# Kernel optimization log

Hardware: AMD Instinct MI355X
Metric: run time of the kernel (lower is better)

The kernel has to match this reference:

```python
import jax, jax.numpy as jnp
import numpy as np

EPS = 1e-6        # RMSNorm140 eps
LAM = 0.1         # lambda_: second-order score weight
HAD = 0.05        # hadamard_scale

def _rmsnorm(x, w):
    return x * jax.lax.rsqrt(jnp.mean(x * x, axis=-1, keepdims=True) + EPS) * w

def _rope(x):
    # x: [b, h, s, d]; interleaved-pair rotary embedding (theta=10000)
    b, h, s, d = x.shape
    inv = 1.0 / (10000.0 ** (jnp.arange(0, d, 2, dtype=jnp.float32) / d))
    ang = jnp.arange(s, dtype=jnp.float32)[:, None] * inv[None, :]  # [s, d/2]
    cos, sin = jnp.cos(ang), jnp.sin(ang)
    x1, x2 = x[..., 0::2], x[..., 1::2]
    out = jnp.stack([x1 * cos - x2 * sin, x1 * sin + x2 * cos], axis=-1)
    return out.reshape(b, h, s, d)

def _rotate_half(x):
    d = x.shape[-1] // 2
    return jnp.concatenate([-x[..., d:], x[..., :d]], axis=-1)

def _attn_pass(Q, K, V):
    # scores = (Q@K^T + lam * Q^2 @ (K^2)^T) / sqrt(head_dim)   (second-order amplify)
    scale = 1.0 / jnp.sqrt(jnp.float32(Q.shape[-1]))
    scores = (jnp.einsum('bhsd,bhtd->bhst', Q, K)
              + LAM * jnp.einsum('bhsd,bhtd->bhst', Q * Q, K * K)) * scale
    return jnp.einsum('bhst,bhtd->bhsd', jax.nn.softmax(scores, axis=-1), V)

def _attention(x, wq, wk, wv, wo, gate_w):
    b, s, dim = x.shape
    hd = gate_w.shape[0]
    nh = dim // hd
    def proj(w):  # StickyLinear: x @ W^T, W stored [out, in]
        return (x @ w.T).reshape(b, s, nh, hd).transpose(0, 2, 1, 3)  # [b,h,s,d]
    Q, K, V = proj(wq), proj(wk), proj(wv)
    Q, K = _rope(Q), _rope(K)
    out1 = _attn_pass(Q, K, V)
    # rotated second pass + per-channel sigmoid gate over head_dim
    out2 = _attn_pass(_rotate_half(Q), _rotate_half(K), V)
    g = jax.nn.sigmoid(gate_w)
    out = out1 * (1.0 - g) + out2 * g
    out = out + HAD * out * out  # Hadamard mix (elementwise nonlinearity)
    out = out.transpose(0, 2, 1, 3).reshape(b, s, dim)
    return out @ wo.T

def _ffn(x, w1, w3, w2):
    # SwiGLU: down( silu(gate(x)) * up(x) )
    return (jax.nn.silu(x @ w1.T) * (x @ w3.T)) @ w2.T

def reference(x, norm1_w, norm2_w, wq, wk, wv, wo, gate_w, w1, w3, w2):
    h = x + _attention(_rmsnorm(x, norm1_w), wq, wk, wv, wo, gate_w)
    return h + _ffn(_rmsnorm(h, norm2_w), w1, w3, w2)

def setup_inputs() -> dict:
    B, S, D, NH, DFF = 2, 1024, 2048, 16, 8192
    HD = D // NH
    key = jax.random.key(0)
    ks = jax.random.split(key, 9)
    std = 0.02
    return {
        'x': jax.random.normal(ks[0], (B, S, D), dtype=jnp.float32),
        'norm1_w': jnp.ones((D,), jnp.float32),
        'norm2_w': jnp.ones((D,), jnp.float32),
        'wq': jax.random.normal(ks[1], (D, D), jnp.float32) * std,
        'wk': jax.random.normal(ks[2], (D, D), jnp.float32) * std,
        'wv': jax.random.normal(ks[3], (D, D), jnp.float32) * std,
        'wo': jax.random.normal(ks[4], (D, D), jnp.float32) * std,
        'gate_w': jax.random.normal(ks[5], (HD,), jnp.float32) * 0.01,
        'w1': jax.random.normal(ks[6], (DFF, D), jnp.float32) * std,
        'w3': jax.random.normal(ks[7], (DFF, D), jnp.float32) * std,
        'w2': jax.random.normal(ks[8], (D, DFF), jnp.float32) * std,
    }
```

## Files before the change

kernel.cpp:

```cpp
#include <hip/hip_runtime.h>
#include <hip/hip_bf16.h>

typedef unsigned short u16;
typedef unsigned int u32;
typedef u16 u16x8 __attribute__((ext_vector_type(8)));
typedef float f32x4 __attribute__((ext_vector_type(4)));

__device__ __forceinline__ u16 f2bf(float f) {
  union { float f; u32 u; } v; v.f = f;
  u32 r = v.u + 0x7FFFu + ((v.u >> 16) & 1u);
  return (u16)(r >> 16);
}
__device__ __forceinline__ float bf2f(u16 h) {
  union { u32 u; float f; } v; v.u = ((u32)h) << 16;
  return v.f;
}
__device__ __forceinline__ void mfma_bf16_16x16x32(f32x4& acc, const f32x4& a, const f32x4& b) {
  asm("v_mfma_f32_16x16x32_bf16 %0, %1, %2, %0" : "+v"(acc) : "v"(a), "v"(b));
}
__device__ __forceinline__ void gload_lds16(const void* g, void* l) {
  __builtin_amdgcn_global_load_lds(
      (const __attribute__((address_space(1))) unsigned int*)g,
      (__attribute__((address_space(3))) unsigned int*)l, 16, 0, 0);
}

__global__ __launch_bounds__(256) void cvt_k(const float* __restrict__ src,
                                             u16* __restrict__ dst, int n8) {
  int i = blockIdx.x * 256 + threadIdx.x;
  if (i >= n8) return;
  float4 f0 = *(const float4*)&src[(size_t)i * 8];
  float4 f1 = *(const float4*)&src[(size_t)i * 8 + 4];
  u16x8 o;
  o[0] = f2bf(f0.x); o[1] = f2bf(f0.y); o[2] = f2bf(f0.z); o[3] = f2bf(f0.w);
  o[4] = f2bf(f1.x); o[5] = f2bf(f1.y); o[6] = f2bf(f1.z); o[7] = f2bf(f1.w);
  *(u16x8*)&dst[(size_t)i * 8] = o;
}

__global__ __launch_bounds__(256) void cvt13_k(const float* __restrict__ src,
                                               u16* __restrict__ dst, int half) {
  int r = blockIdx.x;
  int dr = ((r >> 4) << 5) + (r & 15) + (half << 4);
  int t = threadIdx.x;
  const float* s = src + (size_t)r * 2048 + t * 8;
  float4 f0 = *(const float4*)s;
  float4 f1 = *(const float4*)(s + 4);
  u16x8 o;
  o[0] = f2bf(f0.x); o[1] = f2bf(f0.y); o[2] = f2bf(f0.z); o[3] = f2bf(f0.w);
  o[4] = f2bf(f1.x); o[5] = f2bf(f1.y); o[6] = f2bf(f1.z); o[7] = f2bf(f1.w);
  *(u16x8*)&dst[(size_t)dr * 2048 + t * 8] = o;
}

__global__ __launch_bounds__(256) void rmsnorm_k(const float* __restrict__ X,
                                                 const float* __restrict__ W,
                                                 u16* __restrict__ O) {
  const int row = blockIdx.x;
  const int tid = threadIdx.x;
  const float* x = X + (size_t)row * 2048;
  float4 v0 = *(const float4*)&x[tid * 8];
  float4 v1 = *(const float4*)&x[tid * 8 + 4];
  float s = v0.x * v0.x + v0.y * v0.y + v0.z * v0.z + v0.w * v0.w
          + v1.x * v1.x + v1.y * v1.y + v1.z * v1.z + v1.w * v1.w;
  #pragma unroll
  for (int m = 1; m < 64; m <<= 1) s += __shfl_xor(s, m);
  __shared__ float red[4];
  if ((tid & 63) == 0) red[tid >> 6] = s;
  __syncthreads();
  float tot = red[0] + red[1] + red[2] + red[3];
  float r = rsqrtf(tot * (1.0f / 2048.0f) + 1e-6f);
  float4 w0 = *(const float4*)&W[tid * 8];
  float4 w1 = *(const float4*)&W[tid * 8 + 4];
  u16x8 o;
  o[0] = f2bf(v0.x * r * w0.x); o[1] = f2bf(v0.y * r * w0.y);
  o[2] = f2bf(v0.z * r * w0.z); o[3] = f2bf(v0.w * r * w0.w);
  o[4] = f2bf(v1.x * r * w1.x); o[5] = f2bf(v1.y * r * w1.y);
  o[6] = f2bf(v1.z * r * w1.z); o[7] = f2bf(v1.w * r * w1.w);
  *(u16x8*)&O[(size_t)row * 2048 + tid * 8] = o;
}

#define EPI_F32 0
#define EPI_ADDF32 1
#define EPI_SWIGLU 2
#define EPI_BF16G 3

template <int EPI>
__global__ __launch_bounds__(256) void gemm_bt(const u16* __restrict__ A,
                                               const u16* __restrict__ B,
                                               float* __restrict__ Cf,
                                               u16* __restrict__ Cb,
                                               const float* __restrict__ R,
                                               int M, int N, int Kt,
                                               int lda, int ldb) {
  __shared__ __align__(16) u16 As[2][128 * 32];
  __shared__ __align__(16) u16 Bs[2][128 * 32];
  const int tid = threadIdx.x;
  const int lane = tid & 63;
  const int w = tid >> 6;
  const int wm = w >> 1, wn = w & 1;
  const int m0 = blockIdx.y * 128, n0 = blockIdx.x * 128;
  const int z = blockIdx.z;
  A += (size_t)z * Kt;
  B += (size_t)z * Kt;
  Cf += (size_t)z * M * N;
  const int r0 = tid >> 2;
  const int c0 = (tid & 3) * 8;
  const int r1 = r0 + 64;
  const int laneM = lane & 15;
  const int laneK = (lane >> 4) * 8;

  f32x4 acc[4][4];
  #pragma unroll
  for (int i = 0; i < 4; i++)
    #pragma unroll
    for (int j = 0; j < 4; j++) acc[i][j] = (f32x4){0.f, 0.f, 0.f, 0.f};

  const u16* Ar0 = &A[(size_t)(m0 + r0) * lda + c0];
  const u16* Ar1 = &A[(size_t)(m0 + r1) * lda + c0];
  const u16* Br0 = &B[(size_t)(n0 + r0) * ldb + c0];
  const u16* Br1 = &B[(size_t)(n0 + r1) * ldb + c0];
  const int lofs0 = r0 * 32 + c0;
  const int lofs1 = r1 * 32 + c0;

  auto stage = [&](int bsel, int kt) {
    gload_lds16(Ar0 + kt, &As[bsel][lofs0]);
    gload_lds16(Ar1 + kt, &As[bsel][lofs1]);
    gload_lds16(Br0 + kt, &Bs[bsel][lofs0]);
    gload_lds16(Br1 + kt, &Bs[bsel][lofs1]);
  };

  stage(0, 0);
  const int nt = Kt >> 5;
  for (int t = 0; t < nt; t++) {
    const int cur = t & 1;
    if (t + 1 < nt) {
      stage(cur ^ 1, (t + 1) << 5);
      asm volatile("s_waitcnt vmcnt(4)" ::: "memory");
    } else {
      asm volatile("s_waitcnt vmcnt(0)" ::: "memory");
    }
    __builtin_amdgcn_s_barrier();
    f32x4 af[4], bfr[4];
    #pragma unroll
    for (int mi = 0; mi < 4; mi++)
      af[mi] = *(const f32x4*)&As[cur][(wm * 64 + mi * 16 + laneM) * 32 + laneK];
    #pragma unroll
    for (int ni = 0; ni < 4; ni++)
      bfr[ni] = *(const f32x4*)&Bs[cur][(wn * 64 + ni * 16 + laneM) * 32 + laneK];
    #pragma unroll
    for (int mi = 0; mi < 4; mi++)
      #pragma unroll
      for (int ni = 0; ni < 4; ni++)
        mfma_bf16_16x16x32(acc[mi][ni], af[mi], bfr[ni]);
    __builtin_amdgcn_s_barrier();
  }

  const int rowb = (lane >> 4) * 4;
  const int coll = lane & 15;
  #pragma unroll
  for (int mi = 0; mi < 4; mi++) {
    #pragma unroll
    for (int i = 0; i < 4; i++) {
      int row = m0 + wm * 64 + mi * 16 + rowb + i;
      #pragma unroll
      for (int ni = 0; ni < 4; ni++) {
        int col = n0 + wn * 64 + ni * 16 + coll;
        size_t idx = (size_t)row * N + col;
        float v = acc[mi][ni][i];
        if constexpr (EPI == EPI_F32) Cf[idx] = v;
        else Cf[idx] = v + R[idx];
      }
    }
  }
}

template <int EPI>
__global__ __launch_bounds__(512, 2) void gemm256(const u16* __restrict__ A,
                                                  const u16* __restrict__ B,
                                                  float* __restrict__ Cf,
                                                  u16* __restrict__ Cb,
                                                  int M, int N, int Kt,
                                                  int lda, int ldb) {
  __shared__ __align__(16) char sm[131072];
  const int tid = threadIdx.x;
  const int lane = tid & 63, w = tid >> 6;
  const int wr = w >> 2, wc = w & 3;
  const int laneM = lane & 15, laneG = lane >> 4;
  const int m0 = blockIdx.y * 256, n0 = blockIdx.x * 256;
  const int z = blockIdx.z;
  A += (size_t)z * Kt;
  B += (size_t)z * Kt;
  Cf += (size_t)z * M * N;

  const int srow = tid >> 3;
  const int scb = (tid & 7) * 16;

  f32x4 acc[8][4];
  #pragma unroll
  for (int i = 0; i < 8; i++)
    #pragma unroll
    for (int j = 0; j < 4; j++) acc[i][j] = (f32x4){0.f, 0.f, 0.f, 0.f};

  auto stage = [&](int buf, int ktE, int ht) {
    const int half = ht & 1;
    const bool isA = ht < 2;
    char* base = sm + (isA ? 0 : 65536) + buf * 32768 + half * 16384;
    const u16* src = isA ? A : B;
    const int ld = isA ? lda : ldb;
    const int rb = (isA ? m0 : n0) + half * 128;
    #pragma unroll
    for (int j = 0; j < 2; j++) {
      int row = j * 64 + srow;
      int scol = (scb ^ ((row & 7) << 4)) >> 1;
      gload_lds16(src + (size_t)(rb + row) * ld + ktE + scol,
                  base + j * 8192 + tid * 16);
    }
  };

  const int nkt = Kt >> 6;
  #pragma unroll
  for (int ht = 0; ht < 4; ht++) stage(0, 0, ht);

  const int bHalf = wc >> 1;
  const int bRow0 = (wc & 1) * 64;

  for (int t = 0; t < nkt; t++) {
    const int cb_ = t & 1;
    char* aBase = sm + cb_ * 32768 + wr * 16384;
    char* bBase = sm + 65536 + cb_ * 32768 + bHalf * 16384;
    const bool pre = (t + 1 < nkt);
    const int ktE1 = (t + 1) << 6;

    if (pre) {
      #pragma unroll
      for (int ht = 0; ht < 4; ht++) stage(cb_ ^ 1, ktE1, ht);
      asm volatile("s_waitcnt vmcnt(8)" ::: "memory");
    } else {
      asm volatile("s_waitcnt vmcnt(0)" ::: "memory");
    }
    __builtin_amdgcn_s_barrier();
    __builtin_amdgcn_s_setprio(1);

    f32x4 af[4][2], bg[4][2];
    #pragma unroll
    for (int ni = 0; ni < 4; ni++)
      #pragma unroll
      for (int ks = 0; ks < 2; ks++) {
        int r = bRow0 + ni * 16 + laneM;
        int cbv = ks * 64 + laneG * 16;
        bg[ni][ks] = *(const f32x4*)(bBase + r * 128 + (cbv ^ ((r & 7) << 4)));
      }
    #pragma unroll
    for (int mi = 0; mi < 4; mi++)
      #pragma unroll
      for (int ks = 0; ks < 2; ks++) {
        int r = mi * 16 + laneM;
        int cbv = ks * 64 + laneG * 16;
        af[mi][ks] = *(const f32x4*)(aBase + r * 128 + (cbv ^ ((r & 7) << 4)));
      }
    #pragma unroll
    for (int mi = 0; mi < 4; mi++)
      #pragma unroll
      for (int ni = 0; ni < 4; ni++)
        #pragma unroll
        for (int ks = 0; ks < 2; ks++)
          mfma_bf16_16x16x32(acc[mi][ni], af[mi][ks], bg[ni][ks]);
    #pragma unroll
    for (int mi = 0; mi < 4; mi++)
      #pragma unroll
      for (int ks = 0; ks < 2; ks++) {
        int r = (4 + mi) * 16 + laneM;
        int cbv = ks * 64 + laneG * 16;
        af[mi][ks] = *(const f32x4*)(aBase + r * 128 + (cbv ^ ((r & 7) << 4)));
      }
    #pragma unroll
    for (int mi = 0; mi < 4; mi++)
      #pragma unroll
      for (int ni = 0; ni < 4; ni++)
        #pragma unroll
        for (int ks = 0; ks < 2; ks++)
          mfma_bf16_16x16x32(acc[4 + mi][ni], af[mi][ks], bg[ni][ks]);

    __builtin_amdgcn_s_setprio(0);
    __builtin_amdgcn_s_barrier();
  }

  #pragma unroll
  for (int mi = 0; mi < 8; mi++) {
    #pragma unroll
    for (int i = 0; i < 4; i++) {
      int row = m0 + wr * 128 + mi * 16 + laneG * 4 + i;
      if constexpr (EPI == EPI_SWIGLU) {
        #pragma unroll
        for (int np = 0; np < 2; np++) {
          float g = acc[mi][np * 2][i];
          float u = acc[mi][np * 2 + 1][i];
          float sg = g / (1.0f + __expf(-g));
          int j = (n0 >> 1) + wc * 32 + np * 16 + laneM;
          Cb[(size_t)row * (N >> 1) + j] = f2bf(sg * u);
        }
      } else if constexpr (EPI == EPI_BF16G) {
        #pragma unroll
        for (int ni = 0; ni < 4; ni++) {
          int col = n0 + wc * 64 + ni * 16 + laneM;
          Cb[(size_t)row * N + col] = f2bf(acc[mi][ni][i]);
        }
      } else {
        #pragma unroll
        for (int ni = 0; ni < 4; ni++) {
          int col = n0 + wc * 64 + ni * 16 + laneM;
          Cf[(size_t)row * N + col] = acc[mi][ni][i];
        }
      }
    }
  }
}

__global__ __launch_bounds__(256) void reduce5_k(const float* __restrict__ P,
                                                 const float* __restrict__ H,
                                                 float* __restrict__ out) {
  size_t i = ((size_t)blockIdx.x * 256 + threadIdx.x) * 4;
  const size_t MN = 4194304;
  float4 a = *(const float4*)&P[i];
  float4 b = *(const float4*)&P[MN + i];
  float4 c = *(const float4*)&P[2 * MN + i];
  float4 d = *(const float4*)&P[3 * MN + i];
  float4 h = *(const float4*)&H[i];
  float4 o;
  o.x = a.x + b.x + c.x + d.x + h.x;
  o.y = a.y + b.y + c.y + d.y + h.y;
  o.z = a.z + b.z + c.z + d.z + h.z;
  o.w = a.w + b.w + c.w + d.w + h.w;
  *(float4*)&out[i] = o;
}

__device__ __forceinline__ void rope_row(const u16* __restrict__ src,
                                         u16* __restrict__ dst, int s, int q4) {
  float vv[32];
  #pragma unroll
  for (int t = 0; t < 4; t++) {
    u16x8 v = *(const u16x8*)&src[t * 8];
    #pragma unroll
    for (int j = 0; j < 8; j++) vv[t * 8 + j] = bf2f(v[j]);
  }
  u16 o1[32], o2[32];
  #pragma unroll
  for (int jl = 0; jl < 16; jl++) {
    int j = q4 * 16 + jl;
    float inv = exp2f(-(float)j * 0.20762050593046014f);
    float ang = (float)s * inv;
    float sn, cs;
    __sincosf(ang, &sn, &cs);
    float a = vv[2 * jl], b = vv[2 * jl + 1];
    float r1 = a * cs - b * sn;
    float r2 = a * sn + b * cs;
    o1[2 * jl] = f2bf(r1);
    o1[2 * jl + 1] = f2bf(r2);
    o2[2 * jl] = f2bf(0.31622776601683794f * r1 * r1);
    o2[2 * jl + 1] = f2bf(0.31622776601683794f * r2 * r2);
  }
  #pragma unroll
  for (int t = 0; t < 4; t++) {
    *(u16x8*)&dst[q4 * 32 + t * 8] = *(const u16x8*)&o1[t * 8];
    *(u16x8*)&dst[128 + q4 * 32 + t * 8] = *(const u16x8*)&o2[t * 8];
  }
}

__global__ __launch_bounds__(256) void qkv_post_k(const u16* __restrict__ QKVB,
                                                  u16* __restrict__ Qe,
                                                  u16* __restrict__ Ke,
                                                  u16* __restrict__ Vt) {
  const int st = blockIdx.x;
  const int bh = blockIdx.y;
  const int b = bh >> 4, h = bh & 15;
  const int tid = threadIdx.x;
  {
    int r = tid >> 2, q4 = tid & 3;
    int s = st * 64 + r;
    size_t rowin = ((size_t)b * 1024 + s) * 6144 + h * 128 + q4 * 32;
    size_t rowe = ((size_t)bh * 1024 + s) * 256;
    rope_row(QKVB + rowin, Qe + rowe, s, q4);
    rope_row(QKVB + rowin + 2048, Ke + rowe, s, q4);
  }
  __shared__ __align__(16) u16 vts[128 * 72];
  {
    int r = tid >> 2, q4 = tid & 3;
    int s = st * 64 + r;
    const u16* src = QKVB + ((size_t)b * 1024 + s) * 6144 + 4096 + h * 128 + q4 * 32;
    #pragma unroll
    for (int k = 0; k < 32; k += 8) {
      u16x8 v = *(const u16x8*)&src[k];
      int d = q4 * 32 + k;
      #pragma unroll
      for (int j = 0; j < 8; j++) vts[(d + j) * 72 + r] = v[j];
    }
  }
  __syncthreads();
  {
    int d = tid >> 1, sp = (tid & 1) * 32;
    u16* dst = Vt + ((size_t)bh * 128 + d) * 1024 + st * 64 + sp;
    #pragma unroll
    for (int k = 0; k < 32; k += 8)
      *(u16x8*)&dst[k] = *(const u16x8*)&vts[d * 72 + sp + k];
  }
}

__global__ __launch_bounds__(256, 2) void attn_k(const u16* __restrict__ Qe,
                                                 const u16* __restrict__ Ke,
                                                 const u16* __restrict__ Vt,
                                                 u16* __restrict__ AO) {
  const int bh = blockIdx.x;
  const int qt = blockIdx.y;
  const int b = bh >> 4, h = bh & 15;
  const int tid = threadIdx.x;
  const int w = tid >> 6, lane = tid & 63;
  const int laneM = lane & 15, laneG = lane >> 4;

  __shared__ __align__(16) char smem[57344];
  u16* plu = (u16*)(smem + 49152 + w * 2048);

  const char* KeB = (const char*)Ke + (size_t)bh * 524288;
  const char* VtB = (const char*)Vt + (size_t)bh * 262144;

  const size_t qbase = ((size_t)bh * 1024 + qt * 64 + w * 16 + laneM) * 256 + laneG * 8;
  f32x4 qf[8];
  #pragma unroll
  for (int kk = 0; kk < 8; kk++) qf[kk] = *(const f32x4*)&Qe[qbase + kk * 32];

  float m_i[4], l_i[4];
  #pragma unroll
  for (int i = 0; i < 4; i++) { m_i[i] = -1e30f; l_i[i] = 0.f; }
  f32x4 accO[8];
  #pragma unroll
  for (int n = 0; n < 8; n++) accO[n] = (f32x4){0.f, 0.f, 0.f, 0.f};

  u16x8 kreg[4], vreg[2];
  auto loadRegs = [&](int ktn) {
    const char* ks = KeB + (size_t)ktn * 16384;
    #pragma unroll
    for (int j = 0; j < 4; j++) {
      int p = j * 4096 + tid * 16;
      kreg[j] = *(const u16x8*)(ks + p);
    }
    const char* vs = VtB + (size_t)ktn * 64;
    #pragma unroll
    for (int j = 0; j < 2; j++) {
      int p = j * 4096 + tid * 16;
      int r = p >> 6, x = p & 63;
      vreg[j] = *(const u16x8*)(vs + (size_t)r * 2048 + x);
    }
  };
  auto writeLDS = [&](int bsel) {
    char* kd = smem + (bsel ? 16384 : 0);
    #pragma unroll
    for (int j = 0; j < 4; j++) {
      int p = j * 4096 + tid * 16;
      int r = p >> 9, x = p & 511;
      *(u16x8*)(kd + r * 512 + (x ^ ((r & 7) << 4))) = kreg[j];
    }
    char* vd = smem + 32768 + (bsel ? 8192 : 0);
    #pragma unroll
    for (int j = 0; j < 2; j++) {
      int p = j * 4096 + tid * 16;
      int r = p >> 6, x = p & 63;
      *(u16x8*)(vd + r * 64 + (x ^ (((r >> 1) & 3) << 4))) = vreg[j];
    }
  };

  loadRegs(0);
  writeLDS(0);
  int cur = 0;
  const float scale = 0.08838834764831845f;

  for (int kt = 0; kt < 32; kt++) {
    if (kt < 31) loadRegs(kt + 1);
    __syncthreads();
    const char* Kc = smem + (cur ? 16384 : 0);
    const char* Vc = smem + 32768 + (cur ? 8192 : 0);

    f32x4 accS[2];
    #pragma unroll
    for (int n = 0; n < 2; n++) accS[n] = (f32x4){0.f, 0.f, 0.f, 0.f};
    #pragma unroll
    for (int n = 0; n < 2; n++) {
      int r = n * 16 + laneM;
      const char* krow = Kc + r * 512;
      int sw = (r & 7) << 4;
      #pragma unroll
      for (int kk = 0; kk < 8; kk++) {
        f32x4 kf = *(const f32x4*)(krow + ((kk * 64 + laneG * 16) ^ sw));
        mfma_bf16_16x16x32(accS[n], qf[kk], kf);
      }
    }

    float p[2][4], sf[4];
    #pragma unroll
    for (int i = 0; i < 4; i++) {
      float mx = fmaxf(accS[0][i], accS[1][i]) * scale;
      #pragma unroll
      for (int m = 1; m < 16; m <<= 1) mx = fmaxf(mx, __shfl_xor(mx, m));
      float mnew = fmaxf(m_i[i], mx);
      sf[i] = __expf(m_i[i] - mnew);
      m_i[i] = mnew;
      float p0 = __expf(accS[0][i] * scale - mnew);
      float p1 = __expf(accS[1][i] * scale - mnew);
      p[0][i] = p0; p[1][i] = p1;
      float rs = p0 + p1;
      #pragma unroll
      for (int m = 1; m < 16; m <<= 1) rs += __shfl_xor(rs, m);
      l_i[i] = l_i[i] * sf[i] + rs;
    }
    #pragma unroll
    for (int n = 0; n < 8; n++) {
      accO[n][0] *= sf[0]; accO[n][1] *= sf[1];
      accO[n][2] *= sf[2]; accO[n][3] *= sf[3];
    }

    #pragma unroll
    for (int n = 0; n < 2; n++)
      #pragma unroll
      for (int i = 0; i < 4; i++) {
        int row = laneG * 4 + i;
        int col = n * 16 + laneM;
        plu[row * 64 + (col ^ (((row >> 2) & 3) << 4))] = f2bf(p[n][i]);
      }
    f32x4 pa = *(const f32x4*)&plu[laneM * 64 +
                                   ((laneG * 8) ^ (((laneM >> 2) & 3) << 4))];

    #pragma unroll
    for (int n = 0; n < 8; n++) {
      int r = n * 16 + laneM;
      f32x4 vf = *(const f32x4*)(Vc + r * 64 + ((laneG * 16) ^ (((r >> 1) & 3) << 4)));
      mfma_bf16_16x16x32(accO[n], pa, vf);
    }

    if (kt < 31) writeLDS(cur ^ 1);
    cur ^= 1;
  }

  #pragma unroll
  for (int i = 0; i < 4; i++) {
    float inv_l = 1.f / l_i[i];
    int row = b * 1024 + qt * 64 + w * 16 + laneG * 4 + i;
    #pragma unroll
    for (int n = 0; n < 8; n++) {
      float o = accO[n][i] * inv_l;
      o = o + 0.05f * o * o;
      AO[(size_t)row * 2048 + h * 128 + n * 16 + laneM] = f2bf(o);
    }
  }
}

extern "C" void kernel_launch(void* const* d_in, const int* in_sizes, int n_in,
                              void* d_out, int out_size, void* d_ws, size_t ws_size,
                              hipStream_t stream) {
  const float* x   = (const float*)d_in[0];
  const float* n1w = (const float*)d_in[1];
  const float* n2w = (const float*)d_in[2];
  const float* wq  = (const float*)d_in[3];
  const float* wk  = (const float*)d_in[4];
  const float* wv  = (const float*)d_in[5];
  const float* wo  = (const float*)d_in[6];
  const float* w1  = (const float*)d_in[8];
  const float* w3  = (const float*)d_in[9];
  const float* w2  = (const float*)d_in[10];

  char* ws = (char*)d_ws;
  u16* WQKVb = (u16*)(ws + 0);
  u16* WOb   = (u16*)(ws + 25165824);
  u16* W13b  = (u16*)(ws + 33554432);
  u16* W2b   = (u16*)(ws + 100663296);
  u16* XN    = (u16*)(ws + 134217728);
  u16* QKVB  = (u16*)(ws + 142606336);
  u16* U     = (u16*)(ws + 142606336);
  float* P   = (float*)(ws + 176160768);
  u16* QE    = (u16*)(ws + 192937984);
  u16* KE    = (u16*)(ws + 209715200);
  u16* VT    = (u16*)(ws + 226492416);
  u16* AO    = (u16*)(ws + 234881024);
  float* H   = (float*)(ws + 243269632);

  cvt_k<<<2048, 256, 0, stream>>>(wq, WQKVb, 524288);
  cvt_k<<<2048, 256, 0, stream>>>(wk, WQKVb + 4194304, 524288);
  cvt_k<<<2048, 256, 0, stream>>>(wv, WQKVb + 8388608, 524288);
  cvt_k<<<2048, 256, 0, stream>>>(wo, WOb, 524288);
  cvt13_k<<<8192, 256, 0, stream>>>(w1, W13b, 0);
  cvt13_k<<<8192, 256, 0, stream>>>(w3, W13b, 1);
  cvt_k<<<8192, 256, 0, stream>>>(w2, W2b, 2097152);

  rmsnorm_k<<<2048, 256, 0, stream>>>(x, n1w, XN);

  gemm256<EPI_BF16G><<<dim3(24, 8), 512, 0, stream>>>(
      XN, WQKVb, nullptr, QKVB, 2048, 6144, 2048, 2048, 2048);

  qkv_post_k<<<dim3(16, 32), 256, 0, stream>>>(QKVB, QE, KE, VT);

  attn_k<<<dim3(32, 16), 256, 0, stream>>>(QE, KE, VT, AO);

  gemm_bt<EPI_ADDF32><<<dim3(16, 16), 256, 0, stream>>>(
      AO, WOb, H, nullptr, x, 2048, 2048, 2048, 2048, 2048);

  rmsnorm_k<<<2048, 256, 0, stream>>>(H, n2w, XN);

  gemm256<EPI_SWIGLU><<<dim3(64, 8), 512, 0, stream>>>(
      XN, W13b, nullptr, U, 2048, 16384, 2048, 2048, 2048);

  gemm256<EPI_F32><<<dim3(8, 8, 4), 512, 0, stream>>>(
      U, W2b, P, nullptr, 2048, 2048, 2048, 8192, 8192);

  reduce5_k<<<4096, 256, 0, stream>>>(P, H, (float*)d_out);
}
```

Baseline: 499.1 us.

## Merge weight-conversion launches and split gemm256 prefetch across compute halves

```diff
diff --git a/kernel.cpp b/kernel.cpp
--- a/kernel.cpp
+++ b/kernel.cpp
@@ -24,30 +24,46 @@
       (__attribute__((address_space(3))) unsigned int*)l, 16, 0, 0);
 }
 
+__device__ __forceinline__ u16x8 cvt_row8(const float* p) {
+  float4 f0 = *(const float4*)p;
+  float4 f1 = *(const float4*)(p + 4);
+  u16x8 o;
+  o[0] = f2bf(f0.x); o[1] = f2bf(f0.y); o[2] = f2bf(f0.z); o[3] = f2bf(f0.w);
+  o[4] = f2bf(f1.x); o[5] = f2bf(f1.y); o[6] = f2bf(f1.z); o[7] = f2bf(f1.w);
+  return o;
+}
+
 __global__ __launch_bounds__(256) void cvt_k(const float* __restrict__ src,
                                              u16* __restrict__ dst, int n8) {
   int i = blockIdx.x * 256 + threadIdx.x;
   if (i >= n8) return;
-  float4 f0 = *(const float4*)&src[(size_t)i * 8];
-  float4 f1 = *(const float4*)&src[(size_t)i * 8 + 4];
-  u16x8 o;
-  o[0] = f2bf(f0.x); o[1] = f2bf(f0.y); o[2] = f2bf(f0.z); o[3] = f2bf(f0.w);
-  o[4] = f2bf(f1.x); o[5] = f2bf(f1.y); o[6] = f2bf(f1.z); o[7] = f2bf(f1.w);
-  *(u16x8*)&dst[(size_t)i * 8] = o;
-}
-
-__global__ __launch_bounds__(256) void cvt13_k(const float* __restrict__ src,
-                                               u16* __restrict__ dst, int half) {
-  int r = blockIdx.x;
+  *(u16x8*)&dst[(size_t)i * 8] = cvt_row8(&src[(size_t)i * 8]);
+}
+
+__global__ __launch_bounds__(256) void cvt4_k(const float* __restrict__ s0,
+                                              const float* __restrict__ s1,
+                                              const float* __restrict__ s2,
+                                              const float* __restrict__ s3,
+                                              u16* __restrict__ dst) {
+  int bid = blockIdx.x;
+  const float* s = (bid < 2048) ? s0 : (bid < 4096) ? s1 : (bid < 6144) ? s2 : s3;
+  int r = bid & 2047;
+  int t = threadIdx.x;
+  *(u16x8*)&dst[(size_t)bid * 2048 + t * 8] =
+      cvt_row8(s + (size_t)r * 2048 + t * 8);
+}
+
+__global__ __launch_bounds__(256) void cvt13_2(const float* __restrict__ w1,
+                                               const float* __restrict__ w3,
+                                               u16* __restrict__ dst) {
+  int bid = blockIdx.x;
+  int half = bid >> 13;
+  int r = bid & 8191;
+  const float* s = half ? w3 : w1;
   int dr = ((r >> 4) << 5) + (r & 15) + (half << 4);
   int t = threadIdx.x;
-  const float* s = src + (size_t)r * 2048 + t * 8;
-  float4 f0 = *(const float4*)s;
-  float4 f1 = *(const float4*)(s + 4);
-  u16x8 o;
-  o[0] = f2bf(f0.x); o[1] = f2bf(f0.y); o[2] = f2bf(f0.z); o[3] = f2bf(f0.w);
-  o[4] = f2bf(f1.x); o[5] = f2bf(f1.y); o[6] = f2bf(f1.z); o[7] = f2bf(f1.w);
-  *(u16x8*)&dst[(size_t)dr * 2048 + t * 8] = o;
+  *(u16x8*)&dst[(size_t)dr * 2048 + t * 8] =
+      cvt_row8(s + (size_t)r * 2048 + t * 8);
 }
 
 __global__ __launch_bounds__(256) void rmsnorm_k(const float* __restrict__ X,
@@ -229,17 +245,12 @@
     const bool pre = (t + 1 < nkt);
     const int ktE1 = (t + 1) << 6;
 
-    if (pre) {
-      #pragma unroll
-      for (int ht = 0; ht < 4; ht++) stage(cb_ ^ 1, ktE1, ht);
-      asm volatile("s_waitcnt vmcnt(8)" ::: "memory");
-    } else {
-      asm volatile("s_waitcnt vmcnt(0)" ::: "memory");
-    }
+    f32x4 af[4][2], bg[4][2];
+
+    if (pre) { stage(cb_ ^ 1, ktE1, 0); stage(cb_ ^ 1, ktE1, 1); }
+    if (pre) asm volatile("s_waitcnt vmcnt(4)" ::: "memory");
+    else     asm volatile("s_waitcnt vmcnt(0)" ::: "memory");
     __builtin_amdgcn_s_barrier();
-    __builtin_amdgcn_s_setprio(1);
-
-    f32x4 af[4][2], bg[4][2];
     #pragma unroll
     for (int ni = 0; ni < 4; ni++)
       #pragma unroll
@@ -256,6 +267,9 @@
         int cbv = ks * 64 + laneG * 16;
         af[mi][ks] = *(const f32x4*)(aBase + r * 128 + (cbv ^ ((r & 7) << 4)));
       }
+    asm volatile("s_waitcnt lgkmcnt(0)" ::: "memory");
+    __builtin_amdgcn_sched_barrier(0);
+    __builtin_amdgcn_s_setprio(1);
     #pragma unroll
     for (int mi = 0; mi < 4; mi++)
       #pragma unroll
@@ -263,6 +277,11 @@
         #pragma unroll
         for (int ks = 0; ks < 2; ks++)
           mfma_bf16_16x16x32(acc[mi][ni], af[mi][ks], bg[ni][ks]);
+    __builtin_amdgcn_s_setprio(0);
+    __builtin_amdgcn_sched_barrier(0);
+
+    if (pre) { stage(cb_ ^ 1, ktE1, 2); stage(cb_ ^ 1, ktE1, 3); }
+    __builtin_amdgcn_s_barrier();
     #pragma unroll
     for (int mi = 0; mi < 4; mi++)
       #pragma unroll
@@ -271,6 +290,9 @@
         int cbv = ks * 64 + laneG * 16;
         af[mi][ks] = *(const f32x4*)(aBase + r * 128 + (cbv ^ ((r & 7) << 4)));
       }
+    asm volatile("s_waitcnt lgkmcnt(0)" ::: "memory");
+    __builtin_amdgcn_sched_barrier(0);
+    __builtin_amdgcn_s_setprio(1);
     #pragma unroll
     for (int mi = 0; mi < 4; mi++)
       #pragma unroll
@@ -278,8 +300,8 @@
         #pragma unroll
         for (int ks = 0; ks < 2; ks++)
           mfma_bf16_16x16x32(acc[4 + mi][ni], af[mi][ks], bg[ni][ks]);
-
     __builtin_amdgcn_s_setprio(0);
+    __builtin_amdgcn_sched_barrier(0);
     __builtin_amdgcn_s_barrier();
   }
 
@@ -578,12 +600,8 @@
   u16* AO    = (u16*)(ws + 234881024);
   float* H   = (float*)(ws + 243269632);
 
-  cvt_k<<<2048, 256, 0, stream>>>(wq, WQKVb, 524288);
-  cvt_k<<<2048, 256, 0, stream>>>(wk, WQKVb + 4194304, 524288);
-  cvt_k<<<2048, 256, 0, stream>>>(wv, WQKVb + 8388608, 524288);
-  cvt_k<<<2048, 256, 0, stream>>>(wo, WOb, 524288);
-  cvt13_k<<<8192, 256, 0, stream>>>(w1, W13b, 0);
-  cvt13_k<<<8192, 256, 0, stream>>>(w3, W13b, 1);
+  cvt4_k<<<8192, 256, 0, stream>>>(wq, wk, wv, wo, WQKVb);
+  cvt13_2<<<16384, 256, 0, stream>>>(w1, w3, W13b);
   cvt_k<<<8192, 256, 0, stream>>>(w2, W2b, 2097152);
 
   rmsnorm_k<<<2048, 256, 0, stream>>>(x, n1w, XN);
```

New measurement: 486.9 us. 1.03x faster.
